# Optimization experiments

Measured on AMD Instinct MI355X. Metric: run time of the kernel, lower is better.

The kernel has to match this reference:

```python
import jax, jax.numpy as jnp
import numpy as np

B, S, HID = 1, 2048, 2048
H = 16
Q_LORA, KV_LORA = 768, 512
D_NOPE, D_ROPE, D_V = 128, 64, 128
D_QK = D_NOPE + D_ROPE  # 192
THETA = 10000.0
EPS = 1e-6


def _rms_norm(x, w, eps=EPS):
    var = jnp.mean(x * x, axis=-1, keepdims=True)
    return x * jax.lax.rsqrt(var + eps) * w


def _rotate_half(x):
    # interleaved pairs: (x0,x1,x2,x3,...) -> (-x1,x0,-x3,x2,...)
    x1 = x[..., ::2]
    x2 = x[..., 1::2]
    return jnp.stack((-x2, x1), axis=-1).reshape(x.shape)


def _rope_cache(seq_len, dim, theta=THETA):
    inv_freq = 1.0 / (theta ** (jnp.arange(0, dim, 2, dtype=jnp.float32) / dim))
    pos = jnp.arange(seq_len, dtype=jnp.float32)
    freqs = jnp.outer(pos, inv_freq)          # [S, dim/2]
    emb = jnp.concatenate((freqs, freqs), -1)  # [S, dim]
    return jnp.cos(emb), jnp.sin(emb)


def _apply_rope(x, cos, sin):
    # x: [B, H, S, D]; cos/sin: [S, D]
    cos = cos[None, None]
    sin = sin[None, None]
    return x * cos + _rotate_half(x) * sin


def setup_inputs() -> dict:
    key = jax.random.key(0)
    ks = jax.random.split(key, 8)
    s = lambda fin: 1.0 / np.sqrt(fin)
    return {
        "x": jax.random.normal(ks[0], (B, S, HID), jnp.float32),
        "w_qa": jax.random.normal(ks[1], (HID, Q_LORA), jnp.float32) * s(HID),
        "q_a_norm_w": jnp.ones((Q_LORA,), jnp.float32),
        "w_qb": jax.random.normal(ks[2], (Q_LORA, H * D_QK), jnp.float32) * s(Q_LORA),
        "w_kva": jax.random.normal(ks[3], (HID, KV_LORA + D_ROPE), jnp.float32) * s(HID),
        "kv_a_norm_w": jnp.ones((KV_LORA,), jnp.float32),
        "w_kvb": jax.random.normal(ks[4], (KV_LORA, H * (D_NOPE + D_V)), jnp.float32) * s(KV_LORA),
        "w_o": jax.random.normal(ks[5], (H * D_V, HID), jnp.float32) * s(H * D_V),
    }


def reference(x, w_qa, q_a_norm_w, w_qb, w_kva, kv_a_norm_w, w_kvb, w_o):
    b, seq, _ = x.shape
    # --- query: low-rank down, norm, up ---
    q = _rms_norm(x @ w_qa, q_a_norm_w) @ w_qb           # [B,S,H*D_QK]
    q = q.reshape(b, seq, H, D_QK).transpose(0, 2, 1, 3)  # [B,H,S,D_QK]
    q_nope, q_rope = q[..., :D_NOPE], q[..., D_NOPE:]
    # --- kv: joint low-rank compression + shared rope key ---
    kv = x @ w_kva                                        # [B,S,KV_LORA+D_ROPE]
    c_kv, k_rope = kv[..., :KV_LORA], kv[..., KV_LORA:]
    kv_up = _rms_norm(c_kv, kv_a_norm_w) @ w_kvb          # [B,S,H*(D_NOPE+D_V)]
    kv_up = kv_up.reshape(b, seq, H, D_NOPE + D_V).transpose(0, 2, 1, 3)
    k_nope, v = kv_up[..., :D_NOPE], kv_up[..., D_NOPE:]  # [B,H,S,*]
    # --- decoupled RoPE ---
    cos, sin = _rope_cache(seq, D_ROPE)
    q_rope = _apply_rope(q_rope, cos, sin)
    k_rope = _apply_rope(k_rope[:, None], cos, sin)        # [B,1,S,D_ROPE] shared (MQA)
    k_rope = jnp.broadcast_to(k_rope, (b, H, seq, D_ROPE))
    q_full = jnp.concatenate((q_nope, q_rope), -1)         # [B,H,S,D_QK]
    k_full = jnp.concatenate((k_nope, k_rope), -1)
    # --- causal attention ---
    scale = 1.0 / np.sqrt(D_QK)
    scores = jnp.einsum("bhsd,bhtd->bhst", q_full, k_full) * scale
    mask = jnp.tril(jnp.ones((seq, seq), bool))
    scores = jnp.where(mask[None, None], scores, jnp.finfo(scores.dtype).min)
    attn = jax.nn.softmax(scores, axis=-1)
    out = jnp.einsum("bhst,bhtd->bhsd", attn, v)           # [B,H,S,D_V]
    out = out.transpose(0, 2, 1, 3).reshape(b, seq, H * D_V)
    return out @ w_o
```

## Files before the change

kernel.cpp:

```cpp
#include <hip/hip_runtime.h>
#include <hip/hip_bf16.h>
#include <stdint.h>

typedef __bf16 bf16_t;
typedef bf16_t bf16x8 __attribute__((ext_vector_type(8)));
typedef bf16_t bf16x4 __attribute__((ext_vector_type(4)));
typedef float  f32x4  __attribute__((ext_vector_type(4)));

#define SLEN 2048
#define NHEAD 16

static const size_t OFF_XB    = 0;
static const size_t OFF_WAT   = 8388608;
static const size_t OFF_WQBT  = 14155776;
static const size_t OFF_WKVBT = 18874368;
static const size_t OFF_WOT   = 23068672;
static const size_t OFF_QKVA  = 31457280;
static const size_t OFF_QAN   = 42991616;
static const size_t OFF_CKVN  = 46137344;
static const size_t OFF_COS   = 48234496;
static const size_t OFF_SIN   = 48758784;
static const size_t OFF_QFULL = 49283072;
static const size_t OFF_KFULL = 61865984;
static const size_t OFF_VT    = 74448896;
static const size_t OFF_ATTN  = 82837504;

__device__ __forceinline__ void gll16(const void* g, void* l) {
  __builtin_amdgcn_global_load_lds((__attribute__((address_space(1))) void*)g,
                                   (__attribute__((address_space(3))) void*)l,
                                   16, 0, 0);
}

__global__ __launch_bounds__(256) void k_cvt_bf16(const float* __restrict__ in,
                                                  bf16_t* __restrict__ out, int n) {
  int i = (blockIdx.x * 256 + threadIdx.x) * 8;
  if (i >= n) return;
  f32x4 a = *(const f32x4*)&in[i];
  f32x4 b = *(const f32x4*)&in[i + 4];
  bf16x8 o;
  #pragma unroll
  for (int j = 0; j < 4; j++) { o[j] = (bf16_t)a[j]; o[j + 4] = (bf16_t)b[j]; }
  *(bf16x8*)&out[i] = o;
}

__global__ __launch_bounds__(256) void k_transpose_cvt(const float* __restrict__ in,
                                                       bf16_t* __restrict__ out,
                                                       int K, int N, int Nout) {
  __shared__ float tile[32][33];
  const int nt = blockIdx.x, kt = blockIdx.y;
  const int t = threadIdx.x;
  const int r = t >> 3, c4 = (t & 7) * 4;
  const int gk = kt * 32 + r;
  #pragma unroll
  for (int j = 0; j < 4; j++) {
    int gn = nt * 32 + c4 + j;
    tile[r][c4 + j] = (gn < N) ? in[(size_t)gk * N + gn] : 0.f;
  }
  __syncthreads();
  bf16x4 o;
  #pragma unroll
  for (int j = 0; j < 4; j++) o[j] = (bf16_t)tile[c4 + j][r];
  *(bf16x4*)&out[(size_t)(nt * 32 + r) * K + kt * 32 + c4] = o;
}

__global__ __launch_bounds__(256) void k_rope_tables(float* __restrict__ cosT,
                                                     float* __restrict__ sinT) {
  int i = blockIdx.x * 256 + threadIdx.x;
  int s = i >> 6, d = i & 63;
  float invf = powf(10000.f, -(float)(2 * (d & 31)) / 64.f);
  float ang = (float)s * invf;
  cosT[i] = cosf(ang);
  sinT[i] = sinf(ang);
}

template<int EPI>
__global__ __launch_bounds__(256) void k_gemm(const bf16_t* __restrict__ A,
                                              const bf16_t* __restrict__ Bt,
                                              int M, int N, int K,
                                              float* __restrict__ Cf,
                                              bf16_t* __restrict__ O1,
                                              bf16_t* __restrict__ O2,
                                              const float* __restrict__ cosT,
                                              const float* __restrict__ sinT) {
  __shared__ __align__(16) bf16_t sA[128 * 32];
  __shared__ __align__(16) bf16_t sB[128 * 32];
  const int t = threadIdx.x;
  const int lane = t & 63, wave = t >> 6;
  const int l15 = lane & 15, l4 = lane >> 4;
  const int wr = wave >> 1, wc = wave & 1;
  const int rowBase = blockIdx.y * 128, colBase = blockIdx.x * 128;

  f32x4 acc[4][4] = {};

  const int c0 = t, c1 = t + 256;
  const size_t aoff0 = (size_t)(rowBase + (c0 >> 2)) * K + (c0 & 3) * 8;
  const size_t aoff1 = (size_t)(rowBase + (c1 >> 2)) * K + (c1 & 3) * 8;
  const size_t boff0 = (size_t)(colBase + (c0 >> 2)) * K + (c0 & 3) * 8;
  const size_t boff1 = (size_t)(colBase + (c1 >> 2)) * K + (c1 & 3) * 8;

  for (int k0 = 0; k0 < K; k0 += 32) {
    gll16(A + aoff0 + k0, sA + wave * 512);
    gll16(A + aoff1 + k0, sA + 2048 + wave * 512);
    gll16(Bt + boff0 + k0, sB + wave * 512);
    gll16(Bt + boff1 + k0, sB + 2048 + wave * 512);
    __syncthreads();
    bf16x8 af[4], bfv[4];
    #pragma unroll
    for (int m = 0; m < 4; m++)
      af[m] = *(const bf16x8*)&sA[(wr * 64 + m * 16 + l15) * 32 + l4 * 8];
    #pragma unroll
    for (int n = 0; n < 4; n++)
      bfv[n] = *(const bf16x8*)&sB[(wc * 64 + n * 16 + l15) * 32 + l4 * 8];
    #pragma unroll
    for (int m = 0; m < 4; m++)
      #pragma unroll
      for (int n = 0; n < 4; n++)
        acc[m][n] = __builtin_amdgcn_mfma_f32_16x16x32_bf16(af[m], bfv[n], acc[m][n], 0, 0, 0);
    __syncthreads();
  }

  if (EPI == 0) {
    #pragma unroll
    for (int m = 0; m < 4; m++)
      #pragma unroll
      for (int n = 0; n < 4; n++)
        #pragma unroll
        for (int r = 0; r < 4; r++) {
          int row = rowBase + wr * 64 + m * 16 + l4 * 4 + r;
          int col = colBase + wc * 64 + n * 16 + l15;
          Cf[(size_t)row * N + col] = acc[m][n][r];
        }
  } else if (EPI == 1) {
    #pragma unroll
    for (int m = 0; m < 4; m++)
      #pragma unroll
      for (int n = 0; n < 4; n++) {
        int cb = colBase + wc * 64 + n * 16 + l15;
        int h = cb / 192, d = cb - h * 192;
        #pragma unroll
        for (int r = 0; r < 4; r++) {
          int s = rowBase + wr * 64 + m * 16 + l4 * 4 + r;
          float v = acc[m][n][r];
          float p = __shfl_xor(v, 1);
          float o = v;
          if (d >= 128) {
            int i = d - 128;
            float cs = cosT[s * 64 + i], sn = sinT[s * 64 + i];
            o = (i & 1) ? (v * cs + p * sn) : (v * cs - p * sn);
          }
          O1[((size_t)h * SLEN + s) * 192 + d] = (bf16_t)o;
        }
      }
  } else {
    #pragma unroll
    for (int m = 0; m < 4; m++)
      #pragma unroll
      for (int n = 0; n < 4; n++) {
        int cb = colBase + wc * 64 + n * 16 + l15;
        int h = cb >> 8, w = cb & 255;
        if (w < 128) {
          #pragma unroll
          for (int r = 0; r < 4; r++) {
            int s = rowBase + wr * 64 + m * 16 + l4 * 4 + r;
            O1[((size_t)h * SLEN + s) * 192 + w] = (bf16_t)acc[m][n][r];
          }
        } else {
          int d = w - 128;
          int s0 = rowBase + wr * 64 + m * 16 + l4 * 4;
          bf16x4 o;
          #pragma unroll
          for (int r = 0; r < 4; r++) o[r] = (bf16_t)acc[m][n][r];
          *(bf16x4*)&O2[((size_t)h * 128 + d) * SLEN + s0] = o;
        }
      }
  }
}

__global__ __launch_bounds__(256) void k_rmsnorm_q(const float* __restrict__ qkv,
                                                   const float* __restrict__ w,
                                                   bf16_t* __restrict__ out) {
  __shared__ float red[4];
  const int row = blockIdx.x, t = threadIdx.x;
  const float* x = qkv + (size_t)row * 1408;
  float v0 = x[t], v1 = x[t + 256], v2 = x[t + 512];
  float ss = v0 * v0 + v1 * v1 + v2 * v2;
  #pragma unroll
  for (int off = 32; off; off >>= 1) ss += __shfl_down(ss, off);
  if ((t & 63) == 0) red[t >> 6] = ss;
  __syncthreads();
  ss = red[0] + red[1] + red[2] + red[3];
  float rs = rsqrtf(ss * (1.f / 768.f) + 1e-6f);
  out[(size_t)row * 768 + t]       = (bf16_t)(v0 * rs * w[t]);
  out[(size_t)row * 768 + t + 256] = (bf16_t)(v1 * rs * w[t + 256]);
  out[(size_t)row * 768 + t + 512] = (bf16_t)(v2 * rs * w[t + 512]);
}

__global__ __launch_bounds__(256) void k_rmsnorm_kv(const float* __restrict__ qkv,
                                                    const float* __restrict__ w,
                                                    bf16_t* __restrict__ ckvn,
                                                    bf16_t* __restrict__ kfull,
                                                    const float* __restrict__ cosT,
                                                    const float* __restrict__ sinT) {
  __shared__ float red[4];
  const int row = blockIdx.x, t = threadIdx.x;
  const float* x = qkv + (size_t)row * 1408 + 768;
  float v0 = x[t], v1 = x[t + 256];
  float ss = v0 * v0 + v1 * v1;
  #pragma unroll
  for (int off = 32; off; off >>= 1) ss += __shfl_down(ss, off);
  if ((t & 63) == 0) red[t >> 6] = ss;
  __syncthreads();
  ss = red[0] + red[1] + red[2] + red[3];
  float rs = rsqrtf(ss * (1.f / 512.f) + 1e-6f);
  ckvn[(size_t)row * 512 + t]       = (bf16_t)(v0 * rs * w[t]);
  ckvn[(size_t)row * 512 + t + 256] = (bf16_t)(v1 * rs * w[t + 256]);
  if (t < 64) {
    float xv = x[512 + t];
    float xo = x[512 + (t ^ 1)];
    float cs = cosT[row * 64 + t], sn = sinT[row * 64 + t];
    float o = (t & 1) ? (xv * cs + xo * sn) : (xv * cs - xo * sn);
    bf16_t ob = (bf16_t)o;
    for (int h = 0; h < NHEAD; h++)
      kfull[((size_t)h * SLEN + row) * 192 + 128 + t] = ob;
  }
}

__global__ __launch_bounds__(256) void k_attn(const bf16_t* __restrict__ qfull,
                                              const bf16_t* __restrict__ kfull,
                                              const bf16_t* __restrict__ vT,
                                              bf16_t* __restrict__ out) {
  __shared__ __align__(16) bf16_t sK[2][64 * 192];
  __shared__ __align__(16) bf16_t sV[2][128 * 64];
  __shared__ __align__(16) bf16_t P[4][16][72];
  const int bx = blockIdx.x, h = blockIdx.y;
  const int t = threadIdx.x, lane = t & 63, wave = t >> 6;
  const int l15 = lane & 15, l4 = lane >> 4;
  const bf16_t* qh = qfull + (size_t)h * SLEN * 192;
  const bf16_t* kh = kfull + (size_t)h * SLEN * 192;
  const bf16_t* vh = vT + (size_t)h * 128 * SLEN;

  int koff[6];
  #pragma unroll
  for (int i = 0; i < 6; i++) {
    int D = wave * 6144 + i * 1024 + lane * 16;
    int row = D / 384, cb = D - row * 384;
    koff[i] = row * 192 + ((cb ^ ((row & 7) << 4)) >> 1);
  }
  int voff[4];
  #pragma unroll
  for (int i = 0; i < 4; i++) {
    int D = wave * 4096 + i * 1024 + lane * 16;
    int row = D >> 7, cb = D & 127;
    voff[i] = row * SLEN + ((cb ^ ((row & 7) << 4)) >> 1);
  }
  const int sswz = (l15 & 7) << 4;
  const float scale = 0.0721687836f;

  #pragma unroll 1
  for (int ph = 0; ph < 2; ph++) {
    const int qb = ph ? (31 - bx) : bx;
    const int qr0 = qb * 64 + wave * 16;

    bf16x8 qf[6];
    #pragma unroll
    for (int kk = 0; kk < 6; kk++)
      qf[kk] = *(const bf16x8*)&qh[(size_t)(qr0 + l15) * 192 + kk * 32 + l4 * 8];

    f32x4 oacc[8] = {};
    float mrun[4], lrun[4];
    #pragma unroll
    for (int r = 0; r < 4; r++) { mrun[r] = -3e30f; lrun[r] = 0.f; }
    int rowq[4];
    #pragma unroll
    for (int r = 0; r < 4; r++) rowq[r] = qr0 + l4 * 4 + r;

    #pragma unroll
    for (int i = 0; i < 6; i++)
      gll16(kh + koff[i], (char*)&sK[0][0] + wave * 6144 + i * 1024);
    #pragma unroll
    for (int i = 0; i < 4; i++)
      gll16(vh + voff[i], (char*)&sV[0][0] + wave * 4096 + i * 1024);
    __syncthreads();

    int cur = 0;
    for (int kb = 0; kb <= qb; kb++) {
      const int kv0 = kb * 64;
      if (kb < qb) {
        const bf16_t* ksrc = kh + (size_t)(kv0 + 64) * 192;
        #pragma unroll
        for (int i = 0; i < 6; i++)
          gll16(ksrc + koff[i], (char*)&sK[cur ^ 1][0] + wave * 6144 + i * 1024);
        const bf16_t* vsrc = vh + kv0 + 64;
        #pragma unroll
        for (int i = 0; i < 4; i++)
          gll16(vsrc + voff[i], (char*)&sV[cur ^ 1][0] + wave * 4096 + i * 1024);
      }
      f32x4 sc[4] = {};
      #pragma unroll
      for (int kk = 0; kk < 6; kk++)
        #pragma unroll
        for (int n = 0; n < 4; n++) {
          const bf16_t* p = (const bf16_t*)((const char*)&sK[cur][0] +
                              (n * 16 + l15) * 384 + ((kk * 64 + l4 * 16) ^ sswz));
          bf16x8 bv = *(const bf16x8*)p;
          sc[n] = __builtin_amdgcn_mfma_f32_16x16x32_bf16(qf[kk], bv, sc[n], 0, 0, 0);
        }
      float sv[4][4];
      const bool diag = (kb == qb);
      #pragma unroll
      for (int n = 0; n < 4; n++)
        #pragma unroll
        for (int r = 0; r < 4; r++) {
          float v = sc[n][r] * scale;
          if (diag && (kv0 + n * 16 + l15 > rowq[r])) v = -3e30f;
          sv[n][r] = v;
        }
      float fac[4];
      #pragma unroll
      for (int r = 0; r < 4; r++) {
        float rm = fmaxf(fmaxf(sv[0][r], sv[1][r]), fmaxf(sv[2][r], sv[3][r]));
        #pragma unroll
        for (int off = 1; off < 16; off <<= 1) rm = fmaxf(rm, __shfl_xor(rm, off));
        float mn = fmaxf(mrun[r], rm);
        fac[r] = __expf(mrun[r] - mn);
        mrun[r] = mn;
      }
      float psum[4] = {0.f, 0.f, 0.f, 0.f};
      #pragma unroll
      for (int n = 0; n < 4; n++)
        #pragma unroll
        for (int r = 0; r < 4; r++) {
          float p = __expf(sv[n][r] - mrun[r]);
          psum[r] += p;
          P[wave][l4 * 4 + r][n * 16 + l15] = (bf16_t)p;
        }
      #pragma unroll
      for (int r = 0; r < 4; r++) {
        #pragma unroll
        for (int off = 1; off < 16; off <<= 1) psum[r] += __shfl_xor(psum[r], off);
        lrun[r] = lrun[r] * fac[r] + psum[r];
      }
      #pragma unroll
      for (int n8 = 0; n8 < 8; n8++)
        #pragma unroll
        for (int r = 0; r < 4; r++) oacc[n8][r] *= fac[r];
      #pragma unroll
      for (int kk = 0; kk < 2; kk++) {
        bf16x8 pa = *(const bf16x8*)&P[wave][l15][kk * 32 + l4 * 8];
        #pragma unroll
        for (int n8 = 0; n8 < 8; n8++) {
          const bf16_t* p = (const bf16_t*)((const char*)&sV[cur][0] +
                              (n8 * 16 + l15) * 128 + ((kk * 64 + l4 * 16) ^ sswz));
          bf16x8 vb = *(const bf16x8*)p;
          oacc[n8] = __builtin_amdgcn_mfma_f32_16x16x32_bf16(pa, vb, oacc[n8], 0, 0, 0);
        }
      }
      __syncthreads();
      cur ^= 1;
    }

    #pragma unroll
    for (int n8 = 0; n8 < 8; n8++)
      #pragma unroll
      for (int r = 0; r < 4; r++) {
        int s = qr0 + l4 * 4 + r;
        out[(size_t)s * 2048 + h * 128 + n8 * 16 + l15] = (bf16_t)(oacc[n8][r] / lrun[r]);
      }
  }
}

extern "C" void kernel_launch(void* const* d_in, const int* in_sizes, int n_in,
                              void* d_out, int out_size, void* d_ws, size_t ws_size,
                              hipStream_t stream) {
  const float* x     = (const float*)d_in[0];
  const float* w_qa  = (const float*)d_in[1];
  const float* qnw   = (const float*)d_in[2];
  const float* w_qb  = (const float*)d_in[3];
  const float* w_kva = (const float*)d_in[4];
  const float* kvnw  = (const float*)d_in[5];
  const float* w_kvb = (const float*)d_in[6];
  const float* w_o   = (const float*)d_in[7];
  float* out = (float*)d_out;
  char* ws = (char*)d_ws;

  bf16_t* xb    = (bf16_t*)(ws + OFF_XB);
  bf16_t* wat   = (bf16_t*)(ws + OFF_WAT);
  bf16_t* wqbT  = (bf16_t*)(ws + OFF_WQBT);
  bf16_t* wkvbT = (bf16_t*)(ws + OFF_WKVBT);
  bf16_t* woT   = (bf16_t*)(ws + OFF_WOT);
  float*  qkva  = (float*)(ws + OFF_QKVA);
  bf16_t* qan   = (bf16_t*)(ws + OFF_QAN);
  bf16_t* ckvn  = (bf16_t*)(ws + OFF_CKVN);
  float*  cosT  = (float*)(ws + OFF_COS);
  float*  sinT  = (float*)(ws + OFF_SIN);
  bf16_t* qfull = (bf16_t*)(ws + OFF_QFULL);
  bf16_t* kfull = (bf16_t*)(ws + OFF_KFULL);
  bf16_t* vt    = (bf16_t*)(ws + OFF_VT);
  bf16_t* attn  = (bf16_t*)(ws + OFF_ATTN);

  k_cvt_bf16<<<2048, 256, 0, stream>>>(x, xb, 2048 * 2048);
  k_transpose_cvt<<<dim3(768 / 32, 2048 / 32), 256, 0, stream>>>(w_qa, wat, 2048, 768, 768);
  k_transpose_cvt<<<dim3(640 / 32, 2048 / 32), 256, 0, stream>>>(w_kva, wat + (size_t)768 * 2048, 2048, 576, 640);
  k_transpose_cvt<<<dim3(3072 / 32, 768 / 32), 256, 0, stream>>>(w_qb, wqbT, 768, 3072, 3072);
  k_transpose_cvt<<<dim3(4096 / 32, 512 / 32), 256, 0, stream>>>(w_kvb, wkvbT, 512, 4096, 4096);
  k_transpose_cvt<<<dim3(2048 / 32, 2048 / 32), 256, 0, stream>>>(w_o, woT, 2048, 2048, 2048);
  k_rope_tables<<<2048 * 64 / 256, 256, 0, stream>>>(cosT, sinT);

  k_gemm<0><<<dim3(1408 / 128, 16), 256, 0, stream>>>(xb, wat, 2048, 1408, 2048,
                                                      qkva, nullptr, nullptr, nullptr, nullptr);
  k_rmsnorm_q<<<2048, 256, 0, stream>>>(qkva, qnw, qan);
  k_rmsnorm_kv<<<2048, 256, 0, stream>>>(qkva, kvnw, ckvn, kfull, cosT, sinT);

  k_gemm<1><<<dim3(3072 / 128, 16), 256, 0, stream>>>(qan, wqbT, 2048, 3072, 768,
                                                      nullptr, qfull, nullptr, cosT, sinT);
  k_gemm<2><<<dim3(4096 / 128, 16), 256, 0, stream>>>(ckvn, wkvbT, 2048, 4096, 512,
                                                      nullptr, kfull, vt, nullptr, nullptr);
  k_attn<<<dim3(16, 16), 256, 0, stream>>>(qfull, kfull, vt, attn);
  k_gemm<0><<<dim3(2048 / 128, 16), 256, 0, stream>>>(attn, woT, 2048, 2048, 2048,
                                                      out, nullptr, nullptr, nullptr, nullptr);
}
```

Before: 371.3 us.

## Double-buffer GEMM shared-memory tiles with BK=64 and XOR swizzle

The generic GEMM kernel now uses two shared-memory buffers with a K-tile of 64 instead of a single buffer with 32. It prefetches the next tile via direct global-to-LDS loads while MFMAs run on the current one, and drops one barrier per iteration. The global source addresses are XOR-permuted so that reads into LDS avoid bank conflicts. The cost is four times the LDS footprint (64KB per block), which may reduce occupancy. Correctness relies on the swizzle being consistent between the load addressing and the fragment reads.

New measurement: 340.5 us. 8.3% less time.

```diff
diff --git a/kernel.cpp b/kernel.cpp
--- a/kernel.cpp
+++ b/kernel.cpp
@@ -82,41 +82,64 @@
                                               bf16_t* __restrict__ O2,
                                               const float* __restrict__ cosT,
                                               const float* __restrict__ sinT) {
-  __shared__ __align__(16) bf16_t sA[128 * 32];
-  __shared__ __align__(16) bf16_t sB[128 * 32];
+  __shared__ __align__(16) bf16_t sA[2][128 * 64];
+  __shared__ __align__(16) bf16_t sB[2][128 * 64];
   const int t = threadIdx.x;
   const int lane = t & 63, wave = t >> 6;
   const int l15 = lane & 15, l4 = lane >> 4;
   const int wr = wave >> 1, wc = wave & 1;
   const int rowBase = blockIdx.y * 128, colBase = blockIdx.x * 128;
+  const int sswz = (l15 & 7) << 4;
 
   f32x4 acc[4][4] = {};
 
-  const int c0 = t, c1 = t + 256;
-  const size_t aoff0 = (size_t)(rowBase + (c0 >> 2)) * K + (c0 & 3) * 8;
-  const size_t aoff1 = (size_t)(rowBase + (c1 >> 2)) * K + (c1 & 3) * 8;
-  const size_t boff0 = (size_t)(colBase + (c0 >> 2)) * K + (c0 & 3) * 8;
-  const size_t boff1 = (size_t)(colBase + (c1 >> 2)) * K + (c1 & 3) * 8;
-
-  for (int k0 = 0; k0 < K; k0 += 32) {
-    gll16(A + aoff0 + k0, sA + wave * 512);
-    gll16(A + aoff1 + k0, sA + 2048 + wave * 512);
-    gll16(Bt + boff0 + k0, sB + wave * 512);
-    gll16(Bt + boff1 + k0, sB + 2048 + wave * 512);
+  int soff[4];
+  #pragma unroll
+  for (int i = 0; i < 4; i++) {
+    int D = i * 4096 + t * 16;
+    int row = D >> 7, cb = D & 127;
+    soff[i] = row * K + ((cb ^ ((row & 7) << 4)) >> 1);
+  }
+  const bf16_t* aBase = A + (size_t)rowBase * K;
+  const bf16_t* bBase = Bt + (size_t)colBase * K;
+
+  #pragma unroll
+  for (int i = 0; i < 4; i++) {
+    gll16(aBase + soff[i], (char*)&sA[0][0] + i * 4096 + t * 16);
+    gll16(bBase + soff[i], (char*)&sB[0][0] + i * 4096 + t * 16);
+  }
+  __syncthreads();
+
+  int cur = 0;
+  for (int k0 = 0; k0 < K; k0 += 64) {
+    if (k0 + 64 < K) {
+      #pragma unroll
+      for (int i = 0; i < 4; i++) {
+        gll16(aBase + soff[i] + k0 + 64, (char*)&sA[cur ^ 1][0] + i * 4096 + t * 16);
+        gll16(bBase + soff[i] + k0 + 64, (char*)&sB[cur ^ 1][0] + i * 4096 + t * 16);
+      }
+    }
+    bf16x8 af[4][2], bfv[4][2];
+    #pragma unroll
+    for (int ks = 0; ks < 2; ks++) {
+      #pragma unroll
+      for (int m = 0; m < 4; m++)
+        af[m][ks] = *(const bf16x8*)((const char*)&sA[cur][0] +
+                      (wr * 64 + m * 16 + l15) * 128 + ((ks * 64 + l4 * 16) ^ sswz));
+      #pragma unroll
+      for (int n = 0; n < 4; n++)
+        bfv[n][ks] = *(const bf16x8*)((const char*)&sB[cur][0] +
+                      (wc * 64 + n * 16 + l15) * 128 + ((ks * 64 + l4 * 16) ^ sswz));
+    }
+    #pragma unroll
+    for (int ks = 0; ks < 2; ks++)
+      #pragma unroll
+      for (int m = 0; m < 4; m++)
+        #pragma unroll
+        for (int n = 0; n < 4; n++)
+          acc[m][n] = __builtin_amdgcn_mfma_f32_16x16x32_bf16(af[m][ks], bfv[n][ks], acc[m][n], 0, 0, 0);
     __syncthreads();
-    bf16x8 af[4], bfv[4];
-    #pragma unroll
-    for (int m = 0; m < 4; m++)
-      af[m] = *(const bf16x8*)&sA[(wr * 64 + m * 16 + l15) * 32 + l4 * 8];
-    #pragma unroll
-    for (int n = 0; n < 4; n++)
-      bfv[n] = *(const bf16x8*)&sB[(wc * 64 + n * 16 + l15) * 32 + l4 * 8];
-    #pragma unroll
-    for (int m = 0; m < 4; m++)
-      #pragma unroll
-      for (int n = 0; n < 4; n++)
-        acc[m][n] = __builtin_amdgcn_mfma_f32_16x16x32_bf16(af[m], bfv[n], acc[m][n], 0, 0, 0);
-    __syncthreads();
+    cur ^= 1;
   }
 
   if (EPI == 0) {
```
